# Performance work log

Hardware: AMD Instinct MI355X
Metric: run time of the kernel (lower is better)

## Reference

```python
import jax, jax.numpy as jnp
import numpy as np

D_MODEL = 1024
NUM_HEADS = 16
HEAD_DIM = D_MODEL // NUM_HEADS
SCALE = 1.0 / float(np.sqrt(HEAD_DIM))


def setup_inputs() -> dict:
    key = jax.random.key(0)
    ks = jax.random.split(key, 9)
    B, S, D = 2, 2048, D_MODEL
    # Xavier-uniform bound for square (D, D) linear layers
    bound = float(np.sqrt(6.0 / (D + D)))
    def xavier(k):
        return jax.random.uniform(k, (D, D), jnp.float32, -bound, bound)
    return {
        "x": jax.random.normal(ks[0], (B, S, D), jnp.float32),
        "Wq": xavier(ks[1]), "bq": jnp.zeros((D,), jnp.float32),
        "Wk": xavier(ks[2]), "bk": jnp.zeros((D,), jnp.float32),
        "Wv": xavier(ks[3]), "bv": jnp.zeros((D,), jnp.float32),
        "Wo": xavier(ks[4]), "bo": jnp.zeros((D,), jnp.float32),
    }


def reference(x, Wq, bq, Wk, bk, Wv, bv, Wo, bo):
    B, S, D = x.shape
    H, Hd = NUM_HEADS, HEAD_DIM
    # torch Linear: y = x @ W.T + b
    def proj(W, b):
        y = jnp.einsum("bsd,ed->bse", x, W) + b
        return y.reshape(B, S, H, Hd).transpose(0, 2, 1, 3)  # (B,H,S,Hd)
    Q = proj(Wq, bq)
    K = proj(Wk, bk)
    V = proj(Wv, bv)
    # scaled scores (B,H,S,S) + additive causal mask (0 / -inf)
    scores = jnp.einsum("bhqd,bhkd->bhqk", Q, K) * SCALE
    causal = jnp.where(
        jnp.tril(jnp.ones((S, S), dtype=bool)), 0.0, -jnp.inf
    ).astype(scores.dtype)
    scores = scores + causal
    attn = jax.nn.softmax(scores, axis=-1)
    attn = jnp.nan_to_num(attn, nan=0.0)  # no-op here (causal rows never fully masked)
    # dropout p=0.0 -> identity
    ctx = jnp.einsum("bhqk,bhkd->bhqd", attn, V)  # (B,H,S,Hd)
    ctx = ctx.transpose(0, 2, 1, 3).reshape(B, S, D)
    out = jnp.einsum("bsd,ed->bse", ctx, Wo) + bo
    return out, attn
```

## Files before the change

### kernel.cpp

```cpp
#include <hip/hip_runtime.h>

typedef unsigned short u16;
using short8 = __attribute__((ext_vector_type(8))) short;
using f32x4  = __attribute__((ext_vector_type(4))) float;
using u16x4  = __attribute__((ext_vector_type(4))) unsigned short;

__device__ __forceinline__ u16 f2bf(float f) {
  union { float f; unsigned int u; } v; v.f = f;
  unsigned int u = v.u + 0x7FFFu + ((v.u >> 16) & 1u);
  return (u16)(u >> 16);
}
__device__ __forceinline__ float bf2f(u16 u) {
  union { unsigned int u; float f; } v; v.u = ((unsigned int)u) << 16;
  return v.f;
}
__device__ __forceinline__ void glds16(const void* g, void* l) {
  __builtin_amdgcn_global_load_lds(
      (const __attribute__((address_space(1))) void*)g,
      (__attribute__((address_space(3))) void*)l, 16, 0, 0);
}

__global__ __launch_bounds__(256) void cast_all(
    const float* __restrict__ x, const float* __restrict__ wq,
    const float* __restrict__ wk, const float* __restrict__ wv,
    const float* __restrict__ wo,
    u16* __restrict__ xb, u16* __restrict__ wqb, u16* __restrict__ wkb,
    u16* __restrict__ wvb, u16* __restrict__ wob) {
  int i = blockIdx.x * 256 + threadIdx.x;
  const float4* src; ushort4* dst; int off;
  if (i < 1048576)      { src = (const float4*)x;  dst = (ushort4*)xb;  off = i; }
  else if (i < 1310720) { src = (const float4*)wq; dst = (ushort4*)wqb; off = i - 1048576; }
  else if (i < 1572864) { src = (const float4*)wk; dst = (ushort4*)wkb; off = i - 1310720; }
  else if (i < 1835008) { src = (const float4*)wv; dst = (ushort4*)wvb; off = i - 1572864; }
  else                  { src = (const float4*)wo; dst = (ushort4*)wob; off = i - 1835008; }
  float4 v = src[off];
  ushort4 o;
  o.x = f2bf(v.x); o.y = f2bf(v.y); o.z = f2bf(v.z); o.w = f2bf(v.w);
  dst[off] = o;
}

template<int MODE>
__global__ __launch_bounds__(256) void gemm_nt_glds(
    const u16* __restrict__ A,
    const u16* __restrict__ B0, const u16* __restrict__ B1, const u16* __restrict__ B2,
    const float* __restrict__ bias0, const float* __restrict__ bias1, const float* __restrict__ bias2,
    void* __restrict__ C0, void* __restrict__ C1, void* __restrict__ C2,
    int K)
{
  __shared__ u16 smem[16896];
  u16* As = smem;
  u16* Bs = smem + 8192;
  const int bn = blockIdx.x, bm = blockIdx.y;
  const int sel = bn >> 3, bnl = bn & 7;
  const u16* B = sel == 0 ? B0 : (sel == 1 ? B1 : B2);
  const float* bias = sel == 0 ? bias0 : (sel == 1 ? bias1 : bias2);
  void* C = sel == 0 ? C0 : (sel == 1 ? C1 : C2);

  const int tid = threadIdx.x;
  const int w = tid >> 6, lane = tid & 63, quad = lane >> 4, l16 = lane & 15;
  const int wm = w >> 1, wn = w & 1;
  const int srow = lane >> 3, gc = (lane & 7) ^ srow;

  const u16* aseg = A + (size_t)(bm * 128 + w * 32 + srow) * K + gc * 8;
  const u16* bseg = B + (size_t)(bnl * 128 + w * 32 + srow) * K + gc * 8;

  const f32x4 z4 = {0.f, 0.f, 0.f, 0.f};
  f32x4 acc[4][4];
#pragma unroll
  for (int mt = 0; mt < 4; mt++)
#pragma unroll
    for (int nt = 0; nt < 4; nt++) acc[mt][nt] = z4;

  for (int k0 = 0; k0 < K; k0 += 64) {
    __syncthreads();
#pragma unroll
    for (int j = 0; j < 4; j++) {
      glds16(aseg + (size_t)(j * 8) * K + k0, As + (w * 4 + j) * 512);
      glds16(bseg + (size_t)(j * 8) * K + k0, Bs + (w * 4 + j) * 512);
    }
    __syncthreads();
#pragma unroll
    for (int ks = 0; ks < 2; ks++) {
      short8 af[4], bf[4];
#pragma unroll
      for (int mt = 0; mt < 4; mt++) {
        int row = wm * 64 + mt * 16 + l16;
        int chk = (ks * 4 + quad) ^ (row & 7);
        af[mt] = *(const short8*)((const short*)As + row * 64 + chk * 8);
      }
#pragma unroll
      for (int nt = 0; nt < 4; nt++) {
        int row = wn * 64 + nt * 16 + l16;
        int chk = (ks * 4 + quad) ^ (row & 7);
        bf[nt] = *(const short8*)((const short*)Bs + row * 64 + chk * 8);
      }
#pragma unroll
      for (int mt = 0; mt < 4; mt++)
#pragma unroll
        for (int nt = 0; nt < 4; nt++)
          acc[mt][nt] = __builtin_amdgcn_mfma_f32_16x16x32_bf16(af[mt], bf[nt], acc[mt][nt], 0, 0, 0);
    }
  }

  if (MODE == 0 && sel == 2) {
    __syncthreads();
#pragma unroll
    for (int mt = 0; mt < 4; mt++) {
      int r0 = wm * 64 + mt * 16 + quad * 4;
#pragma unroll
      for (int nt = 0; nt < 4; nt++) {
        int c = wn * 64 + nt * 16 + l16;
        float bvv = bias[bnl * 128 + c];
        u16x4 pk;
#pragma unroll
        for (int r = 0; r < 4; r++) pk[r] = f2bf(acc[mt][nt][r] + bvv);
        *(u16x4*)(smem + c * 132 + r0) = pk;
      }
    }
    __syncthreads();
    const int bb = bm >> 4;
    const size_t sb = (size_t)(bm & 15) * 128;
    u16* Cv = (u16*)C;
#pragma unroll
    for (int i = 0; i < 16; i++) {
      int idx = tid + i * 256;
      int dr = idx >> 5, c4 = (idx & 31) * 4;
      u16x4 v = *(const u16x4*)(smem + dr * 132 + c4);
      *(u16x4*)(Cv + ((size_t)bb * 1024 + bnl * 128 + dr) * 2048 + sb + c4) = v;
    }
  } else {
    const float cmul = (MODE == 0 && sel == 0) ? 0.125f : 1.0f;
#pragma unroll
    for (int mt = 0; mt < 4; mt++) {
      int row0 = bm * 128 + wm * 64 + mt * 16 + quad * 4;
#pragma unroll
      for (int nt = 0; nt < 4; nt++) {
        int col = bnl * 128 + wn * 64 + nt * 16 + l16;
        float bv = bias[col];
#pragma unroll
        for (int r = 0; r < 4; r++) {
          float v = (acc[mt][nt][r] + bv) * cmul;
          if (MODE) ((float*)C)[(size_t)(row0 + r) * 1024 + col] = v;
          else      ((u16*)C)[(size_t)(row0 + r) * 1024 + col] = f2bf(v);
        }
      }
    }
  }
}

__global__ __launch_bounds__(256) void attn_kernel(
    const u16* __restrict__ Qb, const u16* __restrict__ Kbuf,
    const u16* __restrict__ Vtb, float* __restrict__ attn,
    u16* __restrict__ ctx)
{
  __shared__ u16 Ks[2][128 * 64];
  __shared__ u16 Ps[128 * 128];
  __shared__ float ls[128];

  const int flat = blockIdx.x;
  const int x = flat & 7, slot = flat >> 3;
  int bh, qb;
  if (slot < 32) { bh = x * 4 + (slot >> 4);            qb = slot & 15; }
  else           { bh = x * 4 + 2 + ((slot - 32) >> 4); qb = 15 - ((slot - 32) & 15); }
  const int b = bh >> 4, h = bh & 15;

  const int tid = threadIdx.x;
  const int w = tid >> 6, lane = tid & 63, quad = lane >> 4, l16 = lane & 15;
  const int wm = w >> 1, wn = w & 1;
  const int srow8 = lane >> 3, gc8 = (lane & 7) ^ srow8;
  const int srow16 = lane >> 4, sc16 = lane & 15;

  const int S = 2048, D = 1024;
  const u16* Qg = Qb + ((size_t)b * S + qb * 128) * D + h * 64;
  const u16* Kg = Kbuf + (size_t)b * S * D + h * 64;
  const u16* Vg = Vtb + ((size_t)b * D + h * 64) * S;
  float* attng = attn + ((size_t)(b * 16 + h) * S + qb * 128) * S;

  const f32x4 z4 = {0.f, 0.f, 0.f, 0.f};

#pragma unroll
  for (int j = 0; j < 4; j++)
    glds16(Qg + (size_t)(w * 32 + j * 8 + srow8) * D + gc8 * 8, (u16*)Ps + (w * 4 + j) * 512);
  if (tid < 128) ls[tid] = 0.f;
#pragma unroll
  for (int j = 0; j < 4; j++)
    glds16(Kg + (size_t)(w * 32 + j * 8 + srow8) * D + gc8 * 8, Ks[0] + (w * 4 + j) * 512);
  __syncthreads();

  short8 qf[4][2];
#pragma unroll
  for (int mt = 0; mt < 4; mt++) {
    int row = wm * 64 + mt * 16 + l16;
#pragma unroll
    for (int ks = 0; ks < 2; ks++) {
      int chk = (ks * 4 + quad) ^ (row & 7);
      qf[mt][ks] = *(const short8*)((const short*)Ps + row * 64 + chk * 8);
    }
  }

  float rowsum[4][4];
#pragma unroll
  for (int mt = 0; mt < 4; mt++)
#pragma unroll
    for (int rr = 0; rr < 4; rr++) rowsum[mt][rr] = 0.f;

  for (int kb = 0; kb <= qb; kb++) {
    if (kb) __syncthreads();
    if (kb < qb) {
#pragma unroll
      for (int j = 0; j < 4; j++)
        glds16(Kg + (size_t)((kb + 1) * 128 + w * 32 + j * 8 + srow8) * D + gc8 * 8,
               Ks[(kb + 1) & 1] + (w * 4 + j) * 512);
    }
    const u16* kbf = Ks[kb & 1];
    f32x4 acc[4][4];
#pragma unroll
    for (int mt = 0; mt < 4; mt++)
#pragma unroll
      for (int nt = 0; nt < 4; nt++) acc[mt][nt] = z4;
    __builtin_amdgcn_s_setprio(1);
#pragma unroll
    for (int ks = 0; ks < 2; ks++) {
      short8 bf[4];
#pragma unroll
      for (int nt = 0; nt < 4; nt++) {
        int row = wn * 64 + nt * 16 + l16;
        int chk = (ks * 4 + quad) ^ (row & 7);
        bf[nt] = *(const short8*)((const short*)kbf + row * 64 + chk * 8);
      }
#pragma unroll
      for (int mt = 0; mt < 4; mt++)
#pragma unroll
        for (int nt = 0; nt < 4; nt++)
          acc[mt][nt] = __builtin_amdgcn_mfma_f32_16x16x32_bf16(qf[mt][ks], bf[nt], acc[mt][nt], 0, 0, 0);
    }
    __builtin_amdgcn_s_setprio(0);
    if (kb < qb) {
#pragma unroll
      for (int mt = 0; mt < 4; mt++)
#pragma unroll
        for (int rr = 0; rr < 4; rr++) {
          float s = 0.f;
#pragma unroll
          for (int nt = 0; nt < 4; nt++)
            s += __expf(fminf(acc[mt][nt][rr], 30.f));
          rowsum[mt][rr] += s;
        }
    } else {
#pragma unroll
      for (int mt = 0; mt < 4; mt++)
#pragma unroll
        for (int rr = 0; rr < 4; rr++) {
          int rloc = wm * 64 + mt * 16 + quad * 4 + rr;
          float s = 0.f;
#pragma unroll
          for (int nt = 0; nt < 4; nt++) {
            int ck = wn * 64 + nt * 16 + l16;
            s += (ck <= rloc) ? __expf(fminf(acc[mt][nt][rr], 30.f)) : 0.f;
          }
          rowsum[mt][rr] += s;
        }
    }
  }

#pragma unroll
  for (int mt = 0; mt < 4; mt++)
#pragma unroll
    for (int rr = 0; rr < 4; rr++) {
      float s = rowsum[mt][rr];
      s += __shfl_xor(s, 1);
      s += __shfl_xor(s, 2);
      s += __shfl_xor(s, 4);
      s += __shfl_xor(s, 8);
      if (l16 == 0) atomicAdd(&ls[wm * 64 + mt * 16 + quad * 4 + rr], s);
    }
  __syncthreads();
  float rl[4][4];
#pragma unroll
  for (int mt = 0; mt < 4; mt++)
#pragma unroll
    for (int rr = 0; rr < 4; rr++)
      rl[mt][rr] = 1.0f / ls[wm * 64 + mt * 16 + quad * 4 + rr];

#pragma unroll
  for (int j = 0; j < 4; j++)
    glds16(Kg + (size_t)(w * 32 + j * 8 + srow8) * D + gc8 * 8, Ks[0] + (w * 4 + j) * 512);

  f32x4 cacc[2][4];
#pragma unroll
  for (int mt = 0; mt < 2; mt++)
#pragma unroll
    for (int nt = 0; nt < 4; nt++) cacc[mt][nt] = z4;

  for (int kb = 0; kb <= qb; kb++) {
    __syncthreads();
#pragma unroll
    for (int j = 0; j < 4; j++) {
      int r0v = (w * 4 + j) * 4;
      int row = r0v + srow16;
      int gcv = sc16 ^ (row & 7);
      glds16(Vg + (size_t)row * S + kb * 128 + gcv * 8, Ks[1] + r0v * 128);
    }
    f32x4 acc[4][4];
#pragma unroll
    for (int mt = 0; mt < 4; mt++)
#pragma unroll
      for (int nt = 0; nt < 4; nt++) acc[mt][nt] = z4;
    __builtin_amdgcn_s_setprio(1);
#pragma unroll
    for (int ks = 0; ks < 2; ks++) {
      short8 bf[4];
#pragma unroll
      for (int nt = 0; nt < 4; nt++) {
        int row = wn * 64 + nt * 16 + l16;
        int chk = (ks * 4 + quad) ^ (row & 7);
        bf[nt] = *(const short8*)((const short*)Ks[0] + row * 64 + chk * 8);
      }
#pragma unroll
      for (int mt = 0; mt < 4; mt++)
#pragma unroll
        for (int nt = 0; nt < 4; nt++)
          acc[mt][nt] = __builtin_amdgcn_mfma_f32_16x16x32_bf16(qf[mt][ks], bf[nt], acc[mt][nt], 0, 0, 0);
    }
    __builtin_amdgcn_s_setprio(0);
    bool diag = (kb == qb);
#pragma unroll
    for (int mt = 0; mt < 4; mt++)
#pragma unroll
      for (int rr = 0; rr < 4; rr++) {
        int rloc = wm * 64 + mt * 16 + quad * 4 + rr;
        float rlv = rl[mt][rr];
#pragma unroll
        for (int nt = 0; nt < 4; nt++) {
          int colk = wn * 64 + nt * 16 + l16;
          float e = __expf(fminf(acc[mt][nt][rr], 30.f)) * rlv;
          if (diag && colk > rloc) e = 0.f;
          Ps[rloc * 128 + (((colk >> 3) ^ (rloc & 7)) << 3) + (colk & 7)] = f2bf(e);
        }
      }
    __syncthreads();
    if (kb < qb) {
#pragma unroll
      for (int j = 0; j < 4; j++)
        glds16(Kg + (size_t)((kb + 1) * 128 + w * 32 + j * 8 + srow8) * D + gc8 * 8,
               Ks[0] + (w * 4 + j) * 512);
    }
#pragma unroll
    for (int s = 0; s < 16; s++) {
      int e4 = s * 256 + tid;
      int row = e4 >> 5, col = (e4 & 31) * 4;
      int chunk = (col >> 3) ^ (row & 7);
      u16x4 pv = *(const u16x4*)((const u16*)Ps + row * 128 + chunk * 8 + (col & 7));
      f32x4 o;
      o[0] = bf2f(pv[0]); o[1] = bf2f(pv[1]); o[2] = bf2f(pv[2]); o[3] = bf2f(pv[3]);
      __builtin_nontemporal_store(o, (f32x4*)(attng + (size_t)row * S + kb * 128 + col));
    }
    __builtin_amdgcn_s_setprio(1);
#pragma unroll
    for (int ks = 0; ks < 4; ks++) {
      short8 pf[2], vf[4];
#pragma unroll
      for (int mt = 0; mt < 2; mt++) {
        int row = w * 32 + mt * 16 + l16;
        int chk = (ks * 4 + quad) ^ (row & 7);
        pf[mt] = *(const short8*)((const short*)Ps + row * 128 + chk * 8);
      }
#pragma unroll
      for (int nt = 0; nt < 4; nt++) {
        int row = nt * 16 + l16;
        int chk = (ks * 4 + quad) ^ (row & 7);
        vf[nt] = *(const short8*)((const short*)Ks[1] + row * 128 + chk * 8);
      }
#pragma unroll
      for (int mt = 0; mt < 2; mt++)
#pragma unroll
        for (int nt = 0; nt < 4; nt++)
          cacc[mt][nt] = __builtin_amdgcn_mfma_f32_16x16x32_bf16(pf[mt], vf[nt], cacc[mt][nt], 0, 0, 0);
    }
    __builtin_amdgcn_s_setprio(0);
  }

  {
    int kstart = (qb + 1) * 128;
    const f32x4 zz = {0.f, 0.f, 0.f, 0.f};
    for (int rr = 0; rr < 128; rr++) {
      float* rowp = attng + (size_t)rr * S;
      for (int c = kstart + tid * 4; c < S; c += 1024)
        __builtin_nontemporal_store(zz, (f32x4*)(rowp + c));
    }
  }

#pragma unroll
  for (int mt = 0; mt < 2; mt++)
#pragma unroll
    for (int nt = 0; nt < 4; nt++)
#pragma unroll
      for (int rr = 0; rr < 4; rr++) {
        int row_local = w * 32 + mt * 16 + quad * 4 + rr;
        int col = nt * 16 + l16;
        ctx[((size_t)b * S + qb * 128 + row_local) * D + h * 64 + col] = f2bf(cacc[mt][nt][rr]);
      }
}

extern "C" void kernel_launch(void* const* d_in, const int* in_sizes, int n_in,
                              void* d_out, int out_size, void* d_ws, size_t ws_size,
                              hipStream_t stream) {
  const float* x  = (const float*)d_in[0];
  const float* Wq = (const float*)d_in[1];
  const float* bq = (const float*)d_in[2];
  const float* Wk = (const float*)d_in[3];
  const float* bk = (const float*)d_in[4];
  const float* Wv = (const float*)d_in[5];
  const float* bv = (const float*)d_in[6];
  const float* Wo = (const float*)d_in[7];
  const float* bo = (const float*)d_in[8];

  float* out_f32  = (float*)d_out;
  float* attn_out = (float*)d_out + 4194304;

  char* w = (char*)d_ws;
  u16* xb   = (u16*)(w + 0);
  u16* Wqb  = (u16*)(w + 8388608);
  u16* Wkb  = (u16*)(w + 10485760);
  u16* Wvb  = (u16*)(w + 12582912);
  u16* Wob  = (u16*)(w + 14680064);
  u16* Qbuf = (u16*)(w + 16777216);
  u16* Kbuf = (u16*)(w + 25165824);
  u16* Vtb  = (u16*)(w + 41943040);
  u16* ctxb = (u16*)(w + 50331648);

  cast_all<<<8192, 256, 0, stream>>>(x, Wq, Wk, Wv, Wo, xb, Wqb, Wkb, Wvb, Wob);

  gemm_nt_glds<0><<<dim3(24, 32), 256, 0, stream>>>(
      xb, Wqb, Wkb, Wvb, bq, bk, bv, Qbuf, Kbuf, Vtb, 1024);

  attn_kernel<<<512, 256, 0, stream>>>(Qbuf, Kbuf, Vtb, attn_out, ctxb);

  gemm_nt_glds<1><<<dim3(8, 32), 256, 0, stream>>>(
      ctxb, Wob, Wob, Wob, bo, bo, bo, out_f32, out_f32, out_f32, 1024);
}
```

Before: 691.9 us.

## Transpose score MFMA so each lane holds key runs, pack P stores

Swaps the MFMA operands so the score tile is computed as K·Q^T. Each lane then holds four consecutive keys for one query. This lets the probability tile be written to LDS as packed 4-element u16 stores instead of scalar 2-byte stores, and cuts the row-sum reduction to two shuffles per query. It also replaces the per-iteration full __syncthreads in the second pass with a partial vmcnt wait plus a raw barrier, so outstanding global loads can stay in flight. The hand-counted vmcnt(16) is fragile and could race if the number of outstanding loads differs from that count.

```diff
diff --git a/kernel.cpp b/kernel.cpp
--- a/kernel.cpp
+++ b/kernel.cpp
@@ -189,20 +189,18 @@
 
   short8 qf[4][2];
 #pragma unroll
-  for (int mt = 0; mt < 4; mt++) {
-    int row = wm * 64 + mt * 16 + l16;
+  for (int nt = 0; nt < 4; nt++) {
+    int row = wn * 64 + nt * 16 + l16;
 #pragma unroll
     for (int ks = 0; ks < 2; ks++) {
       int chk = (ks * 4 + quad) ^ (row & 7);
-      qf[mt][ks] = *(const short8*)((const short*)Ps + row * 64 + chk * 8);
-    }
-  }
-
-  float rowsum[4][4];
-#pragma unroll
-  for (int mt = 0; mt < 4; mt++)
-#pragma unroll
-    for (int rr = 0; rr < 4; rr++) rowsum[mt][rr] = 0.f;
+      qf[nt][ks] = *(const short8*)((const short*)Ps + row * 64 + chk * 8);
+    }
+  }
+
+  float rowsum[4];
+#pragma unroll
+  for (int nt = 0; nt < 4; nt++) rowsum[nt] = 0.f;
 
   for (int kb = 0; kb <= qb; kb++) {
     if (kb) __syncthreads();
@@ -221,66 +219,60 @@
     __builtin_amdgcn_s_setprio(1);
 #pragma unroll
     for (int ks = 0; ks < 2; ks++) {
-      short8 bf[4];
-#pragma unroll
-      for (int nt = 0; nt < 4; nt++) {
-        int row = wn * 64 + nt * 16 + l16;
-        int chk = (ks * 4 + quad) ^ (row & 7);
-        bf[nt] = *(const short8*)((const short*)kbf + row * 64 + chk * 8);
+      short8 af[4];
+#pragma unroll
+      for (int mt = 0; mt < 4; mt++) {
+        int row = wm * 64 + mt * 16 + l16;
+        int chk = (ks * 4 + quad) ^ (row & 7);
+        af[mt] = *(const short8*)((const short*)kbf + row * 64 + chk * 8);
       }
 #pragma unroll
       for (int mt = 0; mt < 4; mt++)
 #pragma unroll
         for (int nt = 0; nt < 4; nt++)
-          acc[mt][nt] = __builtin_amdgcn_mfma_f32_16x16x32_bf16(qf[mt][ks], bf[nt], acc[mt][nt], 0, 0, 0);
+          acc[mt][nt] = __builtin_amdgcn_mfma_f32_16x16x32_bf16(af[mt], qf[nt][ks], acc[mt][nt], 0, 0, 0);
     }
     __builtin_amdgcn_s_setprio(0);
     if (kb < qb) {
 #pragma unroll
-      for (int mt = 0; mt < 4; mt++)
-#pragma unroll
-        for (int rr = 0; rr < 4; rr++) {
-          float s = 0.f;
-#pragma unroll
-          for (int nt = 0; nt < 4; nt++)
+      for (int nt = 0; nt < 4; nt++) {
+        float s = 0.f;
+#pragma unroll
+        for (int mt = 0; mt < 4; mt++)
+#pragma unroll
+          for (int rr = 0; rr < 4; rr++)
             s += __expf(fminf(acc[mt][nt][rr], 30.f));
-          rowsum[mt][rr] += s;
-        }
+        rowsum[nt] += s;
+      }
     } else {
 #pragma unroll
-      for (int mt = 0; mt < 4; mt++)
-#pragma unroll
-        for (int rr = 0; rr < 4; rr++) {
-          int rloc = wm * 64 + mt * 16 + quad * 4 + rr;
-          float s = 0.f;
-#pragma unroll
-          for (int nt = 0; nt < 4; nt++) {
-            int ck = wn * 64 + nt * 16 + l16;
-            s += (ck <= rloc) ? __expf(fminf(acc[mt][nt][rr], 30.f)) : 0.f;
+      for (int nt = 0; nt < 4; nt++) {
+        int q = wn * 64 + nt * 16 + l16;
+        float s = 0.f;
+#pragma unroll
+        for (int mt = 0; mt < 4; mt++)
+#pragma unroll
+          for (int rr = 0; rr < 4; rr++) {
+            int k = wm * 64 + mt * 16 + quad * 4 + rr;
+            s += (k <= q) ? __expf(fminf(acc[mt][nt][rr], 30.f)) : 0.f;
           }
-          rowsum[mt][rr] += s;
-        }
-    }
-  }
-
-#pragma unroll
-  for (int mt = 0; mt < 4; mt++)
-#pragma unroll
-    for (int rr = 0; rr < 4; rr++) {
-      float s = rowsum[mt][rr];
-      s += __shfl_xor(s, 1);
-      s += __shfl_xor(s, 2);
-      s += __shfl_xor(s, 4);
-      s += __shfl_xor(s, 8);
-      if (l16 == 0) atomicAdd(&ls[wm * 64 + mt * 16 + quad * 4 + rr], s);
-    }
+        rowsum[nt] += s;
+      }
+    }
+  }
+
+#pragma unroll
+  for (int nt = 0; nt < 4; nt++) {
+    float s = rowsum[nt];
+    s += __shfl_xor(s, 16);
+    s += __shfl_xor(s, 32);
+    if (quad == 0) atomicAdd(&ls[wn * 64 + nt * 16 + l16], s);
+  }
   __syncthreads();
-  float rl[4][4];
-#pragma unroll
-  for (int mt = 0; mt < 4; mt++)
-#pragma unroll
-    for (int rr = 0; rr < 4; rr++)
-      rl[mt][rr] = 1.0f / ls[wm * 64 + mt * 16 + quad * 4 + rr];
+  float rl[4];
+#pragma unroll
+  for (int nt = 0; nt < 4; nt++)
+    rl[nt] = 1.0f / ls[wn * 64 + nt * 16 + l16];
 
 #pragma unroll
   for (int j = 0; j < 4; j++)
@@ -293,7 +285,13 @@
     for (int nt = 0; nt < 4; nt++) cacc[mt][nt] = z4;
 
   for (int kb = 0; kb <= qb; kb++) {
-    __syncthreads();
+    if (kb == 0) {
+      __syncthreads();
+    } else {
+      asm volatile("s_waitcnt vmcnt(16)" ::: "memory");
+      __builtin_amdgcn_s_barrier();
+      __builtin_amdgcn_sched_barrier(0);
+    }
 #pragma unroll
     for (int j = 0; j < 4; j++) {
       int r0v = (w * 4 + j) * 4;
@@ -309,35 +307,38 @@
     __builtin_amdgcn_s_setprio(1);
 #pragma unroll
     for (int ks = 0; ks < 2; ks++) {
-      short8 bf[4];
-#pragma unroll
-      for (int nt = 0; nt < 4; nt++) {
-        int row = wn * 64 + nt * 16 + l16;
-        int chk = (ks * 4 + quad) ^ (row & 7);
-        bf[nt] = *(const short8*)((const short*)Ks[0] + row * 64 + chk * 8);
+      short8 af[4];
+#pragma unroll
+      for (int mt = 0; mt < 4; mt++) {
+        int row = wm * 64 + mt * 16 + l16;
+        int chk = (ks * 4 + quad) ^ (row & 7);
+        af[mt] = *(const short8*)((const short*)Ks[0] + row * 64 + chk * 8);
       }
 #pragma unroll
       for (int mt = 0; mt < 4; mt++)
 #pragma unroll
         for (int nt = 0; nt < 4; nt++)
-          acc[mt][nt] = __builtin_amdgcn_mfma_f32_16x16x32_bf16(qf[mt][ks], bf[nt], acc[mt][nt], 0, 0, 0);
+          acc[mt][nt] = __builtin_amdgcn_mfma_f32_16x16x32_bf16(af[mt], qf[nt][ks], acc[mt][nt], 0, 0, 0);
     }
     __builtin_amdgcn_s_setprio(0);
     bool diag = (kb == qb);
 #pragma unroll
-    for (int mt = 0; mt < 4; mt++)
-#pragma unroll
-      for (int rr = 0; rr < 4; rr++) {
-        int rloc = wm * 64 + mt * 16 + quad * 4 + rr;
-        float rlv = rl[mt][rr];
-#pragma unroll
-        for (int nt = 0; nt < 4; nt++) {
-          int colk = wn * 64 + nt * 16 + l16;
+    for (int mt = 0; mt < 4; mt++) {
+      int kbase = wm * 64 + mt * 16 + quad * 4;
+#pragma unroll
+      for (int nt = 0; nt < 4; nt++) {
+        int q = wn * 64 + nt * 16 + l16;
+        float rlv = rl[nt];
+        u16x4 pk;
+#pragma unroll
+        for (int rr = 0; rr < 4; rr++) {
           float e = __expf(fminf(acc[mt][nt][rr], 30.f)) * rlv;
-          if (diag && colk > rloc) e = 0.f;
-          Ps[rloc * 128 + (((colk >> 3) ^ (rloc & 7)) << 3) + (colk & 7)] = f2bf(e);
+          if (diag && (kbase + rr) > q) e = 0.f;
+          pk[rr] = f2bf(e);
         }
-      }
+        *(u16x4*)((u16*)Ps + q * 128 + (((kbase >> 3) ^ (q & 7)) << 3) + (kbase & 7)) = pk;
+      }
+    }
     __syncthreads();
     if (kb < qb) {
 #pragma unroll
```

Measured after the change: 685.8 us. Within noise of the previous version (-0.9%).
